# Performance work log

Measured on AMD Instinct MI355X. Metric: run time of the kernel, lower is better.

The kernel has to match this reference:

```python
import jax, jax.numpy as jnp
import numpy as np

N_NODES = 50000   # n_nodes
N_EDGES = 400000  # n_edges = N_NODES * avg_degree(8)
H = 32            # n_hidden
N_ETYPES = 8      # len(edge_type)
N_LAYER = 3


def setup_inputs() -> dict:
    key = jax.random.key(0)
    ks = jax.random.split(key, 12)
    feature = jax.random.normal(ks[0], (N_NODES, H), dtype=jnp.float32)
    src = jax.random.randint(ks[1], (N_EDGES,), 0, N_NODES, dtype=jnp.int32)
    dst = jax.random.randint(ks[2], (N_EDGES,), 0, N_NODES, dtype=jnp.int32)
    param_id = jax.random.randint(ks[3], (N_EDGES,), 0, N_ETYPES, dtype=jnp.int32)
    # nn.Parameter(...).normal_(): std-1 gaussian per-edge-type weight matrices
    param = jax.random.normal(ks[4], (N_ETYPES, H, H), dtype=jnp.float32)
    # final MLP([H, 2H, 2H, 1]) params (jax convention: weight is (in, out))
    def lin(k, fan_in, fan_out):
        kw, kb = jax.random.split(k)
        bound = 1.0 / np.sqrt(fan_in)
        w = jax.random.uniform(kw, (fan_in, fan_out), jnp.float32, -bound, bound)
        b = jax.random.uniform(kb, (fan_out,), jnp.float32, -bound, bound)
        return w, b
    w1, b1 = lin(ks[5], H, 2 * H)
    w2, b2 = lin(ks[6], 2 * H, 2 * H)
    w3, b3 = lin(ks[7], 2 * H, 1)
    return {"feature": feature, "param": param,
            "w1": w1, "b1": b1, "w2": w2, "b2": b2, "w3": w3, "b3": b3,
            "src": src, "dst": dst, "param_id": param_id}


def reference(feature, param, w1, b1, w2, b2, w3, b3, src, dst, param_id):
    # Edge weights assigned once before the layer loop (as in GNN.forward)
    W = param[param_id]                                  # (E, H, H)
    out = feature                                        # (N, H)
    for _ in range(N_LAYER):
        # message: gather src feats + per-edge matmul ('ei,eij->ej')
        msg = jnp.einsum('ei,eij->ej', out[src], W)      # (E, H)
        # reduce: sum messages into destination nodes
        agg = jax.ops.segment_sum(msg, dst, num_segments=N_NODES)  # (N, H)
        # WeightedConv final output (its internal MLP result is discarded)
        out = (out + agg) * 0.5
    # F.normalize(dim=-1), eps=1e-12
    nrm = jnp.linalg.norm(out, axis=-1, keepdims=True)
    x = out / jnp.maximum(nrm, 1e-12)
    # MLP([H, 2H, 2H, 1]): Linear, Tanh, Linear, Tanh, Linear
    h = jnp.tanh(x @ w1 + b1)
    h = jnp.tanh(h @ w2 + b2)
    logits = (h @ w3 + b3)[..., 0]                       # (N,)
    return jax.nn.sigmoid(logits)
```

## Files before the change

kernel.cpp:

```cpp
#include <hip/hip_runtime.h>
#include <math.h>

#define N_NODES 50000
#define N_EDGES 400000
#define HD 32
#define N_ET 8
#define CAP 64

__device__ inline void fma4(float4& a, float s, const float4 w) {
    a.x = fmaf(s, w.x, a.x);
    a.y = fmaf(s, w.y, a.y);
    a.z = fmaf(s, w.z, a.z);
    a.w = fmaf(s, w.w, a.w);
}

__global__ __launch_bounds__(256) void k_count(
    const int* __restrict__ src, const int* __restrict__ dst,
    const int* __restrict__ pid, int* __restrict__ deg,
    int* __restrict__ payload)
{
    int e = blockIdx.x * blockDim.x + threadIdx.x;
    if (e >= N_EDGES) return;
    int d = dst[e];
    int pos = atomicAdd(&deg[d], 1);
    if (pos < CAP) payload[d * CAP + pos] = pid[e] * N_NODES + src[e];
}

template <int USE_AGG>
__global__ __launch_bounds__(256) void k_transform(
    const float* __restrict__ xin, const float* __restrict__ aggin,
    const float* __restrict__ param, float* __restrict__ cur,
    float* __restrict__ Y)
{
    int n = blockIdx.x * blockDim.x + threadIdx.x;
    if (n >= N_NODES) return;
    const size_t base = (size_t)n * HD;

    float x[HD];
    #pragma unroll
    for (int q = 0; q < 8; ++q) {
        float4 v = *(const float4*)(xin + base + q * 4);
        if (USE_AGG) {
            float4 a = *(const float4*)(aggin + base + q * 4);
            v.x = (v.x + a.x) * 0.5f;
            v.y = (v.y + a.y) * 0.5f;
            v.z = (v.z + a.z) * 0.5f;
            v.w = (v.w + a.w) * 0.5f;
        }
        x[q * 4 + 0] = v.x; x[q * 4 + 1] = v.y;
        x[q * 4 + 2] = v.z; x[q * 4 + 3] = v.w;
        *(float4*)(cur + base + q * 4) = v;
    }

    for (int t = 0; t < N_ET; ++t) {
        const float* W = param + t * (HD * HD);
        float4 acc[8];
        #pragma unroll
        for (int q = 0; q < 8; ++q) acc[q] = make_float4(0.f, 0.f, 0.f, 0.f);
        #pragma unroll
        for (int i = 0; i < HD; ++i) {
            float xi = x[i];
            #pragma unroll
            for (int q = 0; q < 8; ++q)
                fma4(acc[q], xi, *(const float4*)(W + i * HD + q * 4));
        }
        float* yo = Y + (size_t)t * N_NODES * HD + base;
        #pragma unroll
        for (int q = 0; q < 8; ++q) *(float4*)(yo + q * 4) = acc[q];
    }
}

__global__ __launch_bounds__(256) void k_gather(
    const int* __restrict__ deg, const int* __restrict__ payload,
    const float* __restrict__ Y, float* __restrict__ agg)
{
    int tid = blockIdx.x * blockDim.x + threadIdx.x;
    int node = tid >> 3, sl = tid & 7;
    if (node >= N_NODES) return;
    int d = deg[node];
    if (d > CAP) d = CAP;
    const int* pl = payload + node * CAP;
    float4 acc = make_float4(0.f, 0.f, 0.f, 0.f);
    for (int k = 0; k < d; ++k) {
        int c = pl[k];
        const float4 v = *(const float4*)(Y + (size_t)c * HD + sl * 4);
        acc.x += v.x; acc.y += v.y; acc.z += v.z; acc.w += v.w;
    }
    *(float4*)(agg + (size_t)node * HD + sl * 4) = acc;
}

__global__ __launch_bounds__(128) void k_final(
    const float* __restrict__ cur, const float* __restrict__ agg,
    const float* __restrict__ w1, const float* __restrict__ b1,
    const float* __restrict__ w2, const float* __restrict__ b2,
    const float* __restrict__ w3, const float* __restrict__ b3,
    float* __restrict__ out)
{
    __shared__ float xs[128 * 65];
    int n = blockIdx.x * blockDim.x + threadIdx.x;
    if (n >= N_NODES) return;
    float* row = xs + threadIdx.x * 65;
    const size_t base = (size_t)n * HD;

    float ss = 0.f;
    #pragma unroll
    for (int q = 0; q < 8; ++q) {
        float4 a = *(const float4*)(cur + base + q * 4);
        float4 g = *(const float4*)(agg + base + q * 4);
        a.x = (a.x + g.x) * 0.5f; a.y = (a.y + g.y) * 0.5f;
        a.z = (a.z + g.z) * 0.5f; a.w = (a.w + g.w) * 0.5f;
        ss += a.x * a.x + a.y * a.y + a.z * a.z + a.w * a.w;
        row[q * 4 + 0] = a.x; row[q * 4 + 1] = a.y;
        row[q * 4 + 2] = a.z; row[q * 4 + 3] = a.w;
    }
    float rn = 1.0f / fmaxf(sqrtf(ss), 1e-12f);

    float4 h[16];
    #pragma unroll
    for (int q = 0; q < 16; ++q) h[q] = *(const float4*)(b1 + q * 4);
    for (int i = 0; i < HD; ++i) {
        float xi = row[i] * rn;
        #pragma unroll
        for (int q = 0; q < 16; ++q)
            fma4(h[q], xi, *(const float4*)(w1 + i * 64 + q * 4));
    }
    #pragma unroll
    for (int q = 0; q < 16; ++q) {
        row[q * 4 + 0] = tanhf(h[q].x); row[q * 4 + 1] = tanhf(h[q].y);
        row[q * 4 + 2] = tanhf(h[q].z); row[q * 4 + 3] = tanhf(h[q].w);
    }

    float4 h2[16];
    #pragma unroll
    for (int q = 0; q < 16; ++q) h2[q] = *(const float4*)(b2 + q * 4);
    for (int i = 0; i < 64; ++i) {
        float xi = row[i];
        #pragma unroll
        for (int q = 0; q < 16; ++q)
            fma4(h2[q], xi, *(const float4*)(w2 + i * 64 + q * 4));
    }

    float lg = b3[0];
    #pragma unroll
    for (int q = 0; q < 16; ++q) {
        float4 w = *(const float4*)(w3 + q * 4);
        lg = fmaf(tanhf(h2[q].x), w.x, lg);
        lg = fmaf(tanhf(h2[q].y), w.y, lg);
        lg = fmaf(tanhf(h2[q].z), w.z, lg);
        lg = fmaf(tanhf(h2[q].w), w.w, lg);
    }
    out[n] = 1.0f / (1.0f + expf(-lg));
}

extern "C" void kernel_launch(void* const* d_in, const int* in_sizes, int n_in,
                              void* d_out, int out_size, void* d_ws, size_t ws_size,
                              hipStream_t stream) {
    const float* feature = (const float*)d_in[0];
    const float* param   = (const float*)d_in[1];
    const float* w1      = (const float*)d_in[2];
    const float* b1      = (const float*)d_in[3];
    const float* w2      = (const float*)d_in[4];
    const float* b2      = (const float*)d_in[5];
    const float* w3      = (const float*)d_in[6];
    const float* b3      = (const float*)d_in[7];
    const int*   src     = (const int*)d_in[8];
    const int*   dst     = (const int*)d_in[9];
    const int*   pid     = (const int*)d_in[10];
    float* out = (float*)d_out;

    const size_t Y_BYTES   = (size_t)N_ET * N_NODES * HD * sizeof(float);
    const size_t NH_BYTES  = (size_t)N_NODES * HD * sizeof(float);
    const size_t DEG_BYTES = (size_t)N_NODES * sizeof(int);
    char* p = (char*)d_ws;
    float* Y       = (float*)p;            p += Y_BYTES;
    float* cur     = (float*)p;            p += NH_BYTES;
    float* agg     = (float*)p;            p += NH_BYTES;
    int*   deg     = (int*)p;              p += DEG_BYTES;
    int*   payload = (int*)p;

    const int TB = 256;
    const int gT = (N_NODES + TB - 1) / TB;
    const int gE = (N_EDGES + TB - 1) / TB;
    const int gG = (N_NODES * 8 + TB - 1) / TB;
    const int gF = (N_NODES + 127) / 128;

    hipMemsetAsync(deg, 0, DEG_BYTES, stream);
    k_count<<<gE, TB, 0, stream>>>(src, dst, pid, deg, payload);

    k_transform<0><<<gT, TB, 0, stream>>>(feature, nullptr, param, cur, Y);
    k_gather<<<gG, TB, 0, stream>>>(deg, payload, Y, agg);
    k_transform<1><<<gT, TB, 0, stream>>>(cur, agg, param, cur, Y);
    k_gather<<<gG, TB, 0, stream>>>(deg, payload, Y, agg);
    k_transform<1><<<gT, TB, 0, stream>>>(cur, agg, param, cur, Y);
    k_gather<<<gG, TB, 0, stream>>>(deg, payload, Y, agg);
    k_final<<<gF, 128, 0, stream>>>(cur, agg, w1, b1, w2, b2, w3, b3, out);
}
```

Before: 316.3 us.

## Split edge-type transform across grid y and fuse residual update into gather

The per-node transform now launches one block row per edge type (gridDim.y = 8) instead of looping over all 8 types in one thread, which multiplies the parallelism and shortens per-thread work. The residual (x+agg)*0.5 update moves from the start of the next transform into the end of the gather kernel, so the separate agg buffer and its extra read/write are removed. The trade-off is that each transform block rereads the node's input row once per edge type, and the gather now writes its output in place over cur.

```diff
diff --git a/kernel.cpp b/kernel.cpp
--- a/kernel.cpp
+++ b/kernel.cpp
@@ -26,53 +26,43 @@
     if (pos < CAP) payload[d * CAP + pos] = pid[e] * N_NODES + src[e];
 }
 
-template <int USE_AGG>
 __global__ __launch_bounds__(256) void k_transform(
-    const float* __restrict__ xin, const float* __restrict__ aggin,
-    const float* __restrict__ param, float* __restrict__ cur,
+    const float* __restrict__ xin, const float* __restrict__ param,
     float* __restrict__ Y)
 {
     int n = blockIdx.x * blockDim.x + threadIdx.x;
     if (n >= N_NODES) return;
+    const int t = blockIdx.y;
     const size_t base = (size_t)n * HD;
+    const float* W = param + t * (HD * HD);
 
     float x[HD];
     #pragma unroll
     for (int q = 0; q < 8; ++q) {
         float4 v = *(const float4*)(xin + base + q * 4);
-        if (USE_AGG) {
-            float4 a = *(const float4*)(aggin + base + q * 4);
-            v.x = (v.x + a.x) * 0.5f;
-            v.y = (v.y + a.y) * 0.5f;
-            v.z = (v.z + a.z) * 0.5f;
-            v.w = (v.w + a.w) * 0.5f;
-        }
         x[q * 4 + 0] = v.x; x[q * 4 + 1] = v.y;
         x[q * 4 + 2] = v.z; x[q * 4 + 3] = v.w;
-        *(float4*)(cur + base + q * 4) = v;
     }
 
-    for (int t = 0; t < N_ET; ++t) {
-        const float* W = param + t * (HD * HD);
-        float4 acc[8];
+    float4 acc[8];
+    #pragma unroll
+    for (int q = 0; q < 8; ++q) acc[q] = make_float4(0.f, 0.f, 0.f, 0.f);
+    #pragma unroll
+    for (int i = 0; i < HD; ++i) {
+        float xi = x[i];
         #pragma unroll
-        for (int q = 0; q < 8; ++q) acc[q] = make_float4(0.f, 0.f, 0.f, 0.f);
-        #pragma unroll
-        for (int i = 0; i < HD; ++i) {
-            float xi = x[i];
-            #pragma unroll
-            for (int q = 0; q < 8; ++q)
-                fma4(acc[q], xi, *(const float4*)(W + i * HD + q * 4));
-        }
-        float* yo = Y + (size_t)t * N_NODES * HD + base;
-        #pragma unroll
-        for (int q = 0; q < 8; ++q) *(float4*)(yo + q * 4) = acc[q];
+        for (int q = 0; q < 8; ++q)
+            fma4(acc[q], xi, *(const float4*)(W + i * HD + q * 4));
     }
+    float* yo = Y + (size_t)t * N_NODES * HD + base;
+    #pragma unroll
+    for (int q = 0; q < 8; ++q) *(float4*)(yo + q * 4) = acc[q];
 }
 
 __global__ __launch_bounds__(256) void k_gather(
     const int* __restrict__ deg, const int* __restrict__ payload,
-    const float* __restrict__ Y, float* __restrict__ agg)
+    const float* __restrict__ Y, const float* __restrict__ xin,
+    float* __restrict__ xout)
 {
     int tid = blockIdx.x * blockDim.x + threadIdx.x;
     int node = tid >> 3, sl = tid & 7;
@@ -86,11 +76,17 @@
         const float4 v = *(const float4*)(Y + (size_t)c * HD + sl * 4);
         acc.x += v.x; acc.y += v.y; acc.z += v.z; acc.w += v.w;
     }
-    *(float4*)(agg + (size_t)node * HD + sl * 4) = acc;
+    const size_t off = (size_t)node * HD + sl * 4;
+    float4 x = *(const float4*)(xin + off);
+    x.x = (x.x + acc.x) * 0.5f;
+    x.y = (x.y + acc.y) * 0.5f;
+    x.z = (x.z + acc.z) * 0.5f;
+    x.w = (x.w + acc.w) * 0.5f;
+    *(float4*)(xout + off) = x;
 }
 
 __global__ __launch_bounds__(128) void k_final(
-    const float* __restrict__ cur, const float* __restrict__ agg,
+    const float* __restrict__ cur,
     const float* __restrict__ w1, const float* __restrict__ b1,
     const float* __restrict__ w2, const float* __restrict__ b2,
     const float* __restrict__ w3, const float* __restrict__ b3,
@@ -106,9 +102,6 @@
     #pragma unroll
     for (int q = 0; q < 8; ++q) {
         float4 a = *(const float4*)(cur + base + q * 4);
-        float4 g = *(const float4*)(agg + base + q * 4);
-        a.x = (a.x + g.x) * 0.5f; a.y = (a.y + g.y) * 0.5f;
-        a.z = (a.z + g.z) * 0.5f; a.w = (a.w + g.w) * 0.5f;
         ss += a.x * a.x + a.y * a.y + a.z * a.z + a.w * a.w;
         row[q * 4 + 0] = a.x; row[q * 4 + 1] = a.y;
         row[q * 4 + 2] = a.z; row[q * 4 + 3] = a.w;
@@ -174,7 +167,6 @@
     char* p = (char*)d_ws;
     float* Y       = (float*)p;            p += Y_BYTES;
     float* cur     = (float*)p;            p += NH_BYTES;
-    float* agg     = (float*)p;            p += NH_BYTES;
     int*   deg     = (int*)p;              p += DEG_BYTES;
     int*   payload = (int*)p;
 
@@ -183,15 +175,16 @@
     const int gE = (N_EDGES + TB - 1) / TB;
     const int gG = (N_NODES * 8 + TB - 1) / TB;
     const int gF = (N_NODES + 127) / 128;
+    dim3 gridT(gT, N_ET);
 
     hipMemsetAsync(deg, 0, DEG_BYTES, stream);
     k_count<<<gE, TB, 0, stream>>>(src, dst, pid, deg, payload);
 
-    k_transform<0><<<gT, TB, 0, stream>>>(feature, nullptr, param, cur, Y);
-    k_gather<<<gG, TB, 0, stream>>>(deg, payload, Y, agg);
-    k_transform<1><<<gT, TB, 0, stream>>>(cur, agg, param, cur, Y);
-    k_gather<<<gG, TB, 0, stream>>>(deg, payload, Y, agg);
-    k_transform<1><<<gT, TB, 0, stream>>>(cur, agg, param, cur, Y);
-    k_gather<<<gG, TB, 0, stream>>>(deg, payload, Y, agg);
-    k_final<<<gF, 128, 0, stream>>>(cur, agg, w1, b1, w2, b2, w3, b3, out);
+    k_transform<<<gridT, TB, 0, stream>>>(feature, param, Y);
+    k_gather<<<gG, TB, 0, stream>>>(deg, payload, Y, feature, cur);
+    k_transform<<<gridT, TB, 0, stream>>>(cur, param, Y);
+    k_gather<<<gG, TB, 0, stream>>>(deg, payload, Y, cur, cur);
+    k_transform<<<gridT, TB, 0, stream>>>(cur, param, Y);
+    k_gather<<<gG, TB, 0, stream>>>(deg, payload, Y, cur, cur);
+    k_final<<<gF, 128, 0, stream>>>(cur, w1, b1, w2, b2, w3, b3, out);
 }
```

Measured after the change: 266.4 us. 1.19x faster.
